# Performance work log

Measured on AMD Instinct MI355X. Metric: run time of the kernel, lower is better.

## Reference

```python
import jax, jax.numpy as jnp
import numpy as np

D = 1024
H = 16
DFF = 4096
EPS = 1e-5


def layernorm(x, g, b):
    m = jnp.mean(x, axis=-1, keepdims=True)
    v = jnp.var(x, axis=-1, keepdims=True)
    return (x - m) * jax.lax.rsqrt(v + EPS) * g + b


def setup_inputs() -> dict:
    key = jax.random.key(0)
    ks = jax.random.split(key, 6)
    B, T = 2, 2048
    s = 0.02
    return {
        "x": jax.random.normal(ks[0], (B, T, D), dtype=jnp.float32),
        "W_qkv": jax.random.normal(ks[1], (D, 3 * D), dtype=jnp.float32) * s,
        "W_proj": jax.random.normal(ks[2], (D, D), dtype=jnp.float32) * s,
        "W_fc1": jax.random.normal(ks[3], (D, DFF), dtype=jnp.float32) * s,
        "W_fc2": jax.random.normal(ks[4], (DFF, D), dtype=jnp.float32) * s,
        "ln1_g": jnp.ones((D,), jnp.float32),
        "ln1_b": jnp.zeros((D,), jnp.float32),
        "ln2_g": jnp.ones((D,), jnp.float32),
        "ln2_b": jnp.zeros((D,), jnp.float32),
    }


def reference(x, W_qkv, W_proj, W_fc1, W_fc2, ln1_g, ln1_b, ln2_g, ln2_b):
    B, T, C = x.shape
    hd = C // H

    # --- attention sublayer (pre-norm) ---
    h = layernorm(x, ln1_g, ln1_b)
    qkv = h @ W_qkv                                  # [B,T,3C]
    q, k, v = jnp.split(qkv, 3, axis=-1)
    q = q.reshape(B, T, H, hd).transpose(0, 2, 1, 3)  # [B,H,T,hd]
    k = k.reshape(B, T, H, hd).transpose(0, 2, 1, 3)
    v = v.reshape(B, T, H, hd).transpose(0, 2, 1, 3)
    att = jnp.einsum('bhqd,bhkd->bhqk', q, k) * (1.0 / np.sqrt(hd))
    causal = jnp.tril(jnp.ones((T, T), dtype=bool))
    att = jnp.where(causal, att, jnp.float32(-jnp.inf))
    att = jax.nn.softmax(att, axis=-1)
    y = jnp.einsum('bhqk,bhkd->bhqd', att, v)        # [B,H,T,hd]
    y = y.transpose(0, 2, 1, 3).reshape(B, T, C)
    x = x + y @ W_proj

    # --- MLP sublayer (pre-norm) ---
    h = layernorm(x, ln2_g, ln2_b)
    h = jax.nn.gelu(h @ W_fc1, approximate=False)
    x = x + h @ W_fc2
    return x
```

## Files before the change

kernel.cpp:

```cpp
#include <hip/hip_runtime.h>
#include <hip/hip_bf16.h>
#include <math.h>

typedef __bf16 bf16;
typedef __bf16 bf16x4 __attribute__((ext_vector_type(4)));
typedef __bf16 bf16x8 __attribute__((ext_vector_type(8)));
typedef float f32x4 __attribute__((ext_vector_type(4)));
typedef unsigned int u32;

#define MFMA_BF16(a, b, c) __builtin_amdgcn_mfma_f32_16x16x32_bf16(a, b, c, 0, 0, 0)
#define ASYNC16(g, l)                                                                   \
    __builtin_amdgcn_global_load_lds((const __attribute__((address_space(1))) u32*)(g), \
                                     (__attribute__((address_space(3))) u32*)(l), 16, 0, 0)

__global__ __launch_bounds__(256)
void transpose_cast(const float* __restrict__ in, bf16* __restrict__ out, int rows, int cols) {
    __shared__ float tile[32][33];
    const int tx = threadIdx.x, ty = threadIdx.y;
    const int c0 = blockIdx.x * 32, r0 = blockIdx.y * 32;
    #pragma unroll
    for (int j = 0; j < 4; j++)
        tile[ty + j * 8][tx] = in[(size_t)(r0 + ty + j * 8) * cols + c0 + tx];
    __syncthreads();
    #pragma unroll
    for (int j = 0; j < 4; j++)
        out[(size_t)(c0 + ty + j * 8) * rows + r0 + tx] = (bf16)tile[tx][ty + j * 8];
}

__global__ __launch_bounds__(256)
void transpose_v(const bf16* __restrict__ qkv, bf16* __restrict__ vt) {
    __shared__ bf16 tile[32][33];
    const int tx = threadIdx.x, ty = threadIdx.y;
    const int t0 = blockIdx.x * 32;
    const int d0 = blockIdx.y * 32;
    const int bh = blockIdx.z;
    const int b = bh >> 4, h = bh & 15;
    const bf16* src = qkv + (size_t)b * 2048 * 3072 + 2048 + h * 64;
    #pragma unroll
    for (int j = 0; j < 4; j++)
        tile[ty + j * 8][tx] = src[(size_t)(t0 + ty + j * 8) * 3072 + d0 + tx];
    __syncthreads();
    #pragma unroll
    for (int j = 0; j < 4; j++)
        vt[((size_t)bh * 64 + d0 + ty + j * 8) * 2048 + t0 + tx] = tile[tx][ty + j * 8];
}

__global__ __launch_bounds__(256)
void ln_kernel(const float* __restrict__ x, const float* __restrict__ g,
               const float* __restrict__ bb, bf16* __restrict__ out) {
    const int row = blockIdx.x, tid = threadIdx.x;
    const float4 v = reinterpret_cast<const float4*>(x)[(size_t)row * 256 + tid];
    float s = v.x + v.y + v.z + v.w;
    float sq = v.x * v.x + v.y * v.y + v.z * v.z + v.w * v.w;
    #pragma unroll
    for (int o = 32; o > 0; o >>= 1) { s += __shfl_xor(s, o); sq += __shfl_xor(sq, o); }
    __shared__ float ssum[4], ssq[4];
    const int wave = tid >> 6, lane = tid & 63;
    if (lane == 0) { ssum[wave] = s; ssq[wave] = sq; }
    __syncthreads();
    s = ssum[0] + ssum[1] + ssum[2] + ssum[3];
    sq = ssq[0] + ssq[1] + ssq[2] + ssq[3];
    const float mean = s * (1.0f / 1024.0f);
    const float var = sq * (1.0f / 1024.0f) - mean * mean;
    const float rstd = rsqrtf(var + 1e-5f);
    const float4 gv = reinterpret_cast<const float4*>(g)[tid];
    const float4 bv = reinterpret_cast<const float4*>(bb)[tid];
    bf16x4 o;
    o[0] = (bf16)((v.x - mean) * rstd * gv.x + bv.x);
    o[1] = (bf16)((v.y - mean) * rstd * gv.y + bv.y);
    o[2] = (bf16)((v.z - mean) * rstd * gv.z + bv.z);
    o[3] = (bf16)((v.w - mean) * rstd * gv.w + bv.w);
    reinterpret_cast<bf16x4*>(out)[(size_t)row * 256 + tid] = o;
}

__device__ __forceinline__ float gelu_fast(float v) {
    const float vv = v * v;
    const float u = v * (1.595769122f + 0.0713548162726f * vv);
    const float t = exp2f(u * -1.4426950408889634f);
    return v / (1.0f + t);
}

template <int EPI>
__global__ __launch_bounds__(512, 2)
void gemm256(const bf16* __restrict__ A, const bf16* __restrict__ Bt,
             bf16* __restrict__ outb, int M, int N, int K) {
    __shared__ bf16 As[2][2][2][128][32];
    __shared__ bf16 Bs[2][2][2][128][32];
    const int tid = threadIdx.x;
    const int wave = tid >> 6, lane = tid & 63;
    const int lm = lane & 15, lq = lane >> 4;
    const int wr = wave >> 2, wc = wave & 3;
    const int bm = blockIdx.y * 256, bn = blockIdx.x * 256;
    const int srow = lane >> 2;
    const int sg = (((lane & 3) ^ ((lane >> 3) & 3)) * 8);
    const int pco = (lq ^ ((lm >> 1) & 3)) * 8;

    f32x4 acc[8][4];
    #pragma unroll
    for (int i = 0; i < 8; i++)
        #pragma unroll
        for (int j = 0; j < 4; j++) acc[i][j] = (f32x4){0.f, 0.f, 0.f, 0.f};

    auto stageA = [&](int db, int kt) {
        #pragma unroll
        for (int L = 0; L < 2; L++) {
            const int g = wave * 2 + L, slab = g >> 3, rg = g & 7;
            #pragma unroll
            for (int h = 0; h < 2; h++)
                ASYNC16(A + (size_t)(bm + h * 128 + rg * 16 + srow) * K + kt + slab * 32 + sg,
                        &As[db][h][slab][rg * 16][0]);
        }
    };
    auto stageB = [&](int db, int kt) {
        #pragma unroll
        for (int L = 0; L < 2; L++) {
            const int g = wave * 2 + L, slab = g >> 3, rg = g & 7;
            #pragma unroll
            for (int h = 0; h < 2; h++)
                ASYNC16(Bt + (size_t)(bn + h * 128 + rg * 16 + srow) * K + kt + slab * 32 + sg,
                        &Bs[db][h][slab][rg * 16][0]);
        }
    };
    auto loadA = [&](int db, int mq, bf16x8 (&dst)[4][2]) {
        #pragma unroll
        for (int i = 0; i < 4; i++)
            #pragma unroll
            for (int kk = 0; kk < 2; kk++)
                dst[i][kk] = *reinterpret_cast<const bf16x8*>(
                    &As[db][wr][kk][(mq * 4 + i) * 16 + lm][pco]);
    };
    auto loadB = [&](int db, int bq, bf16x8 (&dst)[2][2]) {
        #pragma unroll
        for (int j = 0; j < 2; j++)
            #pragma unroll
            for (int kk = 0; kk < 2; kk++)
                dst[j][kk] = *reinterpret_cast<const bf16x8*>(
                    &Bs[db][wc >> 1][kk][(wc & 1) * 64 + (bq * 2 + j) * 16 + lm][pco]);
    };
    auto quad = [&](int mq, int bq, bf16x8 (&a)[4][2], bf16x8 (&b)[2][2]) {
        #pragma unroll
        for (int kk = 0; kk < 2; kk++)
            #pragma unroll
            for (int i = 0; i < 4; i++)
                #pragma unroll
                for (int j = 0; j < 2; j++)
                    acc[mq * 4 + i][bq * 2 + j] =
                        MFMA_BF16(a[i][kk], b[j][kk], acc[mq * 4 + i][bq * 2 + j]);
    };

#define PHASE_SYNC()                                         \
    __builtin_amdgcn_s_barrier();                            \
    asm volatile("s_waitcnt lgkmcnt(0)" ::: "memory");       \
    __builtin_amdgcn_sched_barrier(0)

    const int NT = K >> 6;
    stageB(0, 0);  stageA(0, 0);
    stageB(1, 64); stageA(1, 64);
    asm volatile("s_waitcnt vmcnt(8)" ::: "memory");
    __builtin_amdgcn_s_barrier();
    __builtin_amdgcn_sched_barrier(0);

    bf16x8 af[4][2], b0[2][2], b1[2][2];
    for (int t = 0; t < NT; ++t) {
        const int db = t & 1;
        const int kt2 = (t + 2) * 64;
        loadA(db, 0, af);
        loadB(db, 0, b0);
        PHASE_SYNC();
        __builtin_amdgcn_s_setprio(1);
        quad(0, 0, af, b0);
        __builtin_amdgcn_s_setprio(0);
        __builtin_amdgcn_s_barrier();
        loadB(db, 1, b1);
        PHASE_SYNC();
        __builtin_amdgcn_s_setprio(1);
        quad(0, 1, af, b1);
        __builtin_amdgcn_s_setprio(0);
        __builtin_amdgcn_s_barrier();
        loadA(db, 1, af);
        if (t + 2 < NT) stageB(db, kt2);
        PHASE_SYNC();
        __builtin_amdgcn_s_setprio(1);
        quad(1, 0, af, b0);
        __builtin_amdgcn_s_setprio(0);
        __builtin_amdgcn_s_barrier();
        if (t + 2 < NT) {
            stageA(db, kt2);
            asm volatile("s_waitcnt vmcnt(8)" ::: "memory");
        } else if (t + 1 < NT) {
            asm volatile("s_waitcnt vmcnt(0)" ::: "memory");
        }
        __builtin_amdgcn_s_barrier();
        __builtin_amdgcn_sched_barrier(0);
        __builtin_amdgcn_s_setprio(1);
        quad(1, 1, af, b1);
        __builtin_amdgcn_s_setprio(0);
        __builtin_amdgcn_s_barrier();
    }
#undef PHASE_SYNC

    const int r0 = bm + wr * 128, c0 = bn + wc * 64;
    #pragma unroll
    for (int mi = 0; mi < 8; mi++)
        #pragma unroll
        for (int ni = 0; ni < 4; ni++)
            #pragma unroll
            for (int e = 0; e < 4; e++) {
                const int row = r0 + mi * 16 + lq * 4 + e;
                const int col = c0 + ni * 16 + lm;
                const float v = acc[mi][ni][e];
                const size_t idx = (size_t)row * N + col;
                if (EPI == 0) outb[idx] = (bf16)v;
                else          outb[idx] = (bf16)gelu_fast(v);
            }
}

__global__ __launch_bounds__(256)
void gemm_bt64(const bf16* __restrict__ A, const bf16* __restrict__ Bt,
               const float* __restrict__ resid, float* __restrict__ outf,
               int M, int N, int K) {
    __shared__ bf16 As[2][128][64];
    __shared__ bf16 Bs[2][64][64];
    const int tid = threadIdx.x;
    const int wave = tid >> 6, lane = tid & 63;
    const int lm = lane & 15, lq = lane >> 4;
    const int wm = (wave >> 1) * 64, wn = (wave & 1) * 32;
    const int bm = blockIdx.y * 128, bn = blockIdx.x * 64;
    const int lr8 = lane >> 3;
    const int lg  = ((lane & 7) ^ lr8) * 8;
    const int sa  = lm & 7;
    int co[2];
    co[0] = (lq ^ sa) * 8;
    co[1] = ((lq ^ 4) ^ sa) * 8;
    f32x4 acc[4][2];
    #pragma unroll
    for (int i = 0; i < 4; i++)
        #pragma unroll
        for (int j = 0; j < 2; j++) acc[i][j] = (f32x4){0.f, 0.f, 0.f, 0.f};

    auto stage = [&](int bb, int kt) {
        #pragma unroll
        for (int s = 0; s < 4; s++)
            ASYNC16(A + (size_t)(bm + wave * 32 + s * 8 + lr8) * K + kt + lg, &As[bb][wave * 32 + s * 8][0]);
        #pragma unroll
        for (int s = 0; s < 2; s++)
            ASYNC16(Bt + (size_t)(bn + wave * 16 + s * 8 + lr8) * K + kt + lg, &Bs[bb][wave * 16 + s * 8][0]);
    };

    stage(0, 0);
    int cur = 0;
    for (int kt = 0; kt < K; kt += 64) {
        __syncthreads();
        if (kt + 64 < K) stage(cur ^ 1, kt + 64);
        bf16x8 af[2][4], bfr[2][2];
        #pragma unroll
        for (int kk = 0; kk < 2; kk++) {
            #pragma unroll
            for (int i = 0; i < 4; i++)
                af[kk][i] = *reinterpret_cast<const bf16x8*>(&As[cur][wm + i * 16 + lm][co[kk]]);
            #pragma unroll
            for (int j = 0; j < 2; j++)
                bfr[kk][j] = *reinterpret_cast<const bf16x8*>(&Bs[cur][wn + j * 16 + lm][co[kk]]);
        }
        #pragma unroll
        for (int kk = 0; kk < 2; kk++)
            #pragma unroll
            for (int i = 0; i < 4; i++)
                #pragma unroll
                for (int j = 0; j < 2; j++)
                    acc[i][j] = MFMA_BF16(af[kk][i], bfr[kk][j], acc[i][j]);
        cur ^= 1;
    }

    const int r0 = bm + wm, c0 = bn + wn;
    #pragma unroll
    for (int i = 0; i < 4; i++)
        #pragma unroll
        for (int j = 0; j < 2; j++)
            #pragma unroll
            for (int e = 0; e < 4; e++) {
                const int row = r0 + i * 16 + lq * 4 + e;
                const int col = c0 + j * 16 + lm;
                const size_t idx = (size_t)row * N + col;
                outf[idx] = resid[idx] + acc[i][j][e];
            }
}

__global__ __launch_bounds__(256)
void attn_kernel(const bf16* __restrict__ qkv, const bf16* __restrict__ vt,
                 bf16* __restrict__ y) {
    __shared__ bf16 Ks[64][68];
    __shared__ bf16 Vt[64][68];
    __shared__ bf16 Ps[4][16][68];
    const int tid = threadIdx.x, wave = tid >> 6, lane = tid & 63;
    const int lm = lane & 15, lq = lane >> 4;
    const int h = blockIdx.y, b = blockIdx.z;
    const size_t base = (size_t)b * 2048 * 3072;
    const bf16* Kbase = qkv + base + 1024 + h * 64;
    const bf16* Vbase = vt + ((size_t)(b * 16 + h) * 64) * 2048;
    const int skey = tid >> 3, sch = (tid & 7) * 8;
    const float k1 = 0.18033688011112042f;

    bf16x8 ones;
    #pragma unroll
    for (int j = 0; j < 8; j++) ones[j] = (lm == 0) ? (bf16)1.0f : (bf16)0.0f;

    for (int ph = 0; ph < 2; ph++) {
        const int qt = ph ? (int)blockIdx.x : 31 - (int)blockIdx.x;

        const int qrow = qt * 64 + wave * 16 + lm;
        const bf16* qp = qkv + base + (size_t)qrow * 3072 + h * 64 + lq * 8;
        bf16x8 aq0 = *reinterpret_cast<const bf16x8*>(qp);
        bf16x8 aq1 = *reinterpret_cast<const bf16x8*>(qp + 32);
        #pragma unroll
        for (int j = 0; j < 8; j++) {
            aq0[j] = (bf16)((float)aq0[j] * k1);
            aq1[j] = (bf16)((float)aq1[j] * k1);
        }

        f32x4 Oc[4], Ol;
        #pragma unroll
        for (int nt = 0; nt < 4; nt++) Oc[nt] = (f32x4){0.f, 0.f, 0.f, 0.f};
        Ol = (f32x4){0.f, 0.f, 0.f, 0.f};

        bf16x8 pk0, pk1, pv0, pv1;
        {
            const bf16* kp = Kbase + (size_t)skey * 3072 + sch;
            pk0 = *reinterpret_cast<const bf16x8*>(kp);
            pk1 = *reinterpret_cast<const bf16x8*>(kp + (size_t)32 * 3072);
            const bf16* vp = Vbase + (size_t)skey * 2048 + sch;
            pv0 = *reinterpret_cast<const bf16x8*>(vp);
            pv1 = *reinterpret_cast<const bf16x8*>(vp + (size_t)32 * 2048);
        }

        for (int kt2 = 0; kt2 <= qt; kt2++) {
            __syncthreads();
            *reinterpret_cast<bf16x8*>(&Ks[skey][sch])      = pk0;
            *reinterpret_cast<bf16x8*>(&Ks[skey + 32][sch]) = pk1;
            *reinterpret_cast<bf16x8*>(&Vt[skey][sch])      = pv0;
            *reinterpret_cast<bf16x8*>(&Vt[skey + 32][sch]) = pv1;
            __syncthreads();
            if (kt2 < qt) {
                const bf16* kp = Kbase + (size_t)((kt2 + 1) * 64 + skey) * 3072 + sch;
                pk0 = *reinterpret_cast<const bf16x8*>(kp);
                pk1 = *reinterpret_cast<const bf16x8*>(kp + (size_t)32 * 3072);
                const bf16* vp = Vbase + (size_t)skey * 2048 + (kt2 + 1) * 64 + sch;
                pv0 = *reinterpret_cast<const bf16x8*>(vp);
                pv1 = *reinterpret_cast<const bf16x8*>(vp + (size_t)32 * 2048);
            }

            f32x4 Sc[4];
            #pragma unroll
            for (int nt = 0; nt < 4; nt++) Sc[nt] = (f32x4){0.f, 0.f, 0.f, 0.f};
            #pragma unroll
            for (int nt = 0; nt < 4; nt++) {
                const bf16x8 bk0 = *reinterpret_cast<const bf16x8*>(&Ks[nt * 16 + lm][lq * 8]);
                const bf16x8 bk1 = *reinterpret_cast<const bf16x8*>(&Ks[nt * 16 + lm][32 + lq * 8]);
                Sc[nt] = MFMA_BF16(aq0, bk0, Sc[nt]);
                Sc[nt] = MFMA_BF16(aq1, bk1, Sc[nt]);
            }

            const int qb = wave * 16 + lq * 4;
            #pragma unroll
            for (int e = 0; e < 4; e++) {
                #pragma unroll
                for (int nt = 0; nt < 4; nt++) {
                    float sv = Sc[nt][e];
                    if (kt2 == qt && (nt * 16 + lm) > (qb + e)) sv = -1e30f;
                    Ps[wave][lq * 4 + e][nt * 16 + lm] = (bf16)exp2f(sv);
                }
            }

            const bf16x8 ap0 = *reinterpret_cast<const bf16x8*>(&Ps[wave][lm][lq * 8]);
            const bf16x8 ap1 = *reinterpret_cast<const bf16x8*>(&Ps[wave][lm][32 + lq * 8]);
            Ol = MFMA_BF16(ap0, ones, Ol);
            Ol = MFMA_BF16(ap1, ones, Ol);
            #pragma unroll
            for (int nt = 0; nt < 4; nt++) {
                const bf16x8 bv0 = *reinterpret_cast<const bf16x8*>(&Vt[nt * 16 + lm][lq * 8]);
                const bf16x8 bv1 = *reinterpret_cast<const bf16x8*>(&Vt[nt * 16 + lm][32 + lq * 8]);
                Oc[nt] = MFMA_BF16(ap0, bv0, Oc[nt]);
                Oc[nt] = MFMA_BF16(ap1, bv1, Oc[nt]);
            }
        }

        const int qrow0 = qt * 64 + wave * 16 + lq * 4;
        float inv[4];
        #pragma unroll
        for (int e = 0; e < 4; e++) inv[e] = 1.0f / __shfl(Ol[e], lane & 48);
        #pragma unroll
        for (int nt = 0; nt < 4; nt++)
            #pragma unroll
            for (int e = 0; e < 4; e++) {
                const int row = qrow0 + e;
                y[((size_t)b * 2048 + row) * 1024 + h * 64 + nt * 16 + lm] = (bf16)(Oc[nt][e] * inv[e]);
            }
    }
}

extern "C" void kernel_launch(void* const* d_in, const int* in_sizes, int n_in,
                              void* d_out, int out_size, void* d_ws, size_t ws_size,
                              hipStream_t stream) {
    const float* x     = (const float*)d_in[0];
    const float* Wqkv  = (const float*)d_in[1];
    const float* Wproj = (const float*)d_in[2];
    const float* Wfc1  = (const float*)d_in[3];
    const float* Wfc2  = (const float*)d_in[4];
    const float* ln1g  = (const float*)d_in[5];
    const float* ln1b  = (const float*)d_in[6];
    const float* ln2g  = (const float*)d_in[7];
    const float* ln2b  = (const float*)d_in[8];
    float* out = (float*)d_out;
    char* ws = (char*)d_ws;

    bf16*  Wqkvt  = (bf16*)(ws);
    bf16*  Wprojt = (bf16*)(ws + 6291456);
    bf16*  Wfc1t  = (bf16*)(ws + 8388608);
    bf16*  Wfc2t  = (bf16*)(ws + 16777216);
    bf16*  hb     = (bf16*)(ws + 25165824);
    bf16*  vt     = (bf16*)(ws + 25165824);
    bf16*  qkv    = (bf16*)(ws + 33554432);
    bf16*  yb     = (bf16*)(ws + 58720256);
    float* x1     = (float*)(ws + 67108864);
    bf16*  h3     = (bf16*)(ws + 33554432);

    const dim3 tb(32, 8);
    transpose_cast<<<dim3(96, 32), tb, 0, stream>>>(Wqkv, Wqkvt, 1024, 3072);
    transpose_cast<<<dim3(32, 32), tb, 0, stream>>>(Wproj, Wprojt, 1024, 1024);
    transpose_cast<<<dim3(128, 32), tb, 0, stream>>>(Wfc1, Wfc1t, 1024, 4096);
    transpose_cast<<<dim3(32, 128), tb, 0, stream>>>(Wfc2, Wfc2t, 4096, 1024);

    ln_kernel<<<dim3(4096), dim3(256), 0, stream>>>(x, ln1g, ln1b, hb);
    gemm256<0><<<dim3(12, 16), dim3(512), 0, stream>>>(hb, Wqkvt, qkv, 4096, 3072, 1024);
    transpose_v<<<dim3(64, 2, 32), tb, 0, stream>>>(qkv, vt);
    attn_kernel<<<dim3(16, 16, 2), dim3(256), 0, stream>>>(qkv, vt, yb);
    gemm_bt64<<<dim3(16, 32), dim3(256), 0, stream>>>(yb, Wprojt, x, x1, 4096, 1024, 1024);
    ln_kernel<<<dim3(4096), dim3(256), 0, stream>>>(x1, ln2g, ln2b, hb);
    gemm256<2><<<dim3(16, 16), dim3(512), 0, stream>>>(hb, Wfc1t, h3, 4096, 4096, 1024);
    gemm_bt64<<<dim3(16, 32), dim3(256), 0, stream>>>(h3, Wfc2t, x1, out, 4096, 1024, 4096);
}
```

Baseline: 343.3 us.

## Replace residual GEMM with 128x128 tile, K=32 steps and swizzled block order

The residual-add GEMMs (projection and fc2) move from a 128x64 tile with K-step 64 to a 128x128 tile with K-step 32. Each wave now computes a 64x64 sub-tile with 16 accumulators, which raises MFMA work per LDS fragment load. The grid halves to 256 workgroups, and block indices are remapped in groups of 8 (likely to improve L2 locality). The LDS swizzle is redone for the 32-wide rows. Fewer workgroups (256) on a large-CU GPU may leave compute units idle, and the shorter K step adds more barriers per unit of work.

```diff
diff --git a/kernel.cpp b/kernel.cpp
--- a/kernel.cpp
+++ b/kernel.cpp
@@ -216,59 +216,54 @@
 }
 
 __global__ __launch_bounds__(256)
-void gemm_bt64(const bf16* __restrict__ A, const bf16* __restrict__ Bt,
-               const float* __restrict__ resid, float* __restrict__ outf,
-               int M, int N, int K) {
-    __shared__ bf16 As[2][128][64];
-    __shared__ bf16 Bs[2][64][64];
+void gemm128r(const bf16* __restrict__ A, const bf16* __restrict__ Bt,
+              const float* __restrict__ resid, float* __restrict__ outf,
+              int M, int N, int K) {
+    __shared__ bf16 As[2][128][32];
+    __shared__ bf16 Bs[2][128][32];
     const int tid = threadIdx.x;
     const int wave = tid >> 6, lane = tid & 63;
     const int lm = lane & 15, lq = lane >> 4;
-    const int wm = (wave >> 1) * 64, wn = (wave & 1) * 32;
-    const int bm = blockIdx.y * 128, bn = blockIdx.x * 64;
-    const int lr8 = lane >> 3;
-    const int lg  = ((lane & 7) ^ lr8) * 8;
-    const int sa  = lm & 7;
-    int co[2];
-    co[0] = (lq ^ sa) * 8;
-    co[1] = ((lq ^ 4) ^ sa) * 8;
-    f32x4 acc[4][2];
+    const int wm = (wave >> 1) * 64, wn = (wave & 1) * 64;
+    const int nwg = gridDim.x * gridDim.y;
+    const int orig = blockIdx.x + gridDim.x * blockIdx.y;
+    const int cpx = nwg >> 3;
+    const int swz = (orig & 7) * cpx + (orig >> 3);
+    const int bx = swz % gridDim.x, by = swz / gridDim.x;
+    const int bm = by * 128, bn = bx * 128;
+    const int srow = lane >> 2;
+    const int sg = (((lane & 3) ^ ((lane >> 3) & 3)) * 8);
+    const int pco = (lq ^ ((lm >> 1) & 3)) * 8;
+    f32x4 acc[4][4];
     #pragma unroll
     for (int i = 0; i < 4; i++)
         #pragma unroll
-        for (int j = 0; j < 2; j++) acc[i][j] = (f32x4){0.f, 0.f, 0.f, 0.f};
+        for (int j = 0; j < 4; j++) acc[i][j] = (f32x4){0.f, 0.f, 0.f, 0.f};
 
     auto stage = [&](int bb, int kt) {
-        #pragma unroll
-        for (int s = 0; s < 4; s++)
-            ASYNC16(A + (size_t)(bm + wave * 32 + s * 8 + lr8) * K + kt + lg, &As[bb][wave * 32 + s * 8][0]);
-        #pragma unroll
-        for (int s = 0; s < 2; s++)
-            ASYNC16(Bt + (size_t)(bn + wave * 16 + s * 8 + lr8) * K + kt + lg, &Bs[bb][wave * 16 + s * 8][0]);
+        ASYNC16(A + (size_t)(bm + wave * 32 + srow) * K + kt + sg,      &As[bb][wave * 32][0]);
+        ASYNC16(A + (size_t)(bm + wave * 32 + 16 + srow) * K + kt + sg, &As[bb][wave * 32 + 16][0]);
+        ASYNC16(Bt + (size_t)(bn + wave * 32 + srow) * K + kt + sg,      &Bs[bb][wave * 32][0]);
+        ASYNC16(Bt + (size_t)(bn + wave * 32 + 16 + srow) * K + kt + sg, &Bs[bb][wave * 32 + 16][0]);
     };
 
     stage(0, 0);
     int cur = 0;
-    for (int kt = 0; kt < K; kt += 64) {
+    for (int kt = 0; kt < K; kt += 32) {
         __syncthreads();
-        if (kt + 64 < K) stage(cur ^ 1, kt + 64);
-        bf16x8 af[2][4], bfr[2][2];
-        #pragma unroll
-        for (int kk = 0; kk < 2; kk++) {
-            #pragma unroll
-            for (int i = 0; i < 4; i++)
-                af[kk][i] = *reinterpret_cast<const bf16x8*>(&As[cur][wm + i * 16 + lm][co[kk]]);
-            #pragma unroll
-            for (int j = 0; j < 2; j++)
-                bfr[kk][j] = *reinterpret_cast<const bf16x8*>(&Bs[cur][wn + j * 16 + lm][co[kk]]);
-        }
-        #pragma unroll
-        for (int kk = 0; kk < 2; kk++)
-            #pragma unroll
-            for (int i = 0; i < 4; i++)
-                #pragma unroll
-                for (int j = 0; j < 2; j++)
-                    acc[i][j] = MFMA_BF16(af[kk][i], bfr[kk][j], acc[i][j]);
+        if (kt + 32 < K) stage(cur ^ 1, kt + 32);
+        bf16x8 af[4], bfr[4];
+        #pragma unroll
+        for (int i = 0; i < 4; i++)
+            af[i] = *reinterpret_cast<const bf16x8*>(&As[cur][wm + i * 16 + lm][pco]);
+        #pragma unroll
+        for (int j = 0; j < 4; j++)
+            bfr[j] = *reinterpret_cast<const bf16x8*>(&Bs[cur][wn + j * 16 + lm][pco]);
+        #pragma unroll
+        for (int i = 0; i < 4; i++)
+            #pragma unroll
+            for (int j = 0; j < 4; j++)
+                acc[i][j] = MFMA_BF16(af[i], bfr[j], acc[i][j]);
         cur ^= 1;
     }
 
@@ -276,7 +271,7 @@
     #pragma unroll
     for (int i = 0; i < 4; i++)
         #pragma unroll
-        for (int j = 0; j < 2; j++)
+        for (int j = 0; j < 4; j++)
             #pragma unroll
             for (int e = 0; e < 4; e++) {
                 const int row = r0 + i * 16 + lq * 4 + e;
@@ -434,8 +429,8 @@
     gemm256<0><<<dim3(12, 16), dim3(512), 0, stream>>>(hb, Wqkvt, qkv, 4096, 3072, 1024);
     transpose_v<<<dim3(64, 2, 32), tb, 0, stream>>>(qkv, vt);
     attn_kernel<<<dim3(16, 16, 2), dim3(256), 0, stream>>>(qkv, vt, yb);
-    gemm_bt64<<<dim3(16, 32), dim3(256), 0, stream>>>(yb, Wprojt, x, x1, 4096, 1024, 1024);
+    gemm128r<<<dim3(8, 32), dim3(256), 0, stream>>>(yb, Wprojt, x, x1, 4096, 1024, 1024);
     ln_kernel<<<dim3(4096), dim3(256), 0, stream>>>(x1, ln2g, ln2b, hb);
     gemm256<2><<<dim3(16, 16), dim3(512), 0, stream>>>(hb, Wfc1t, h3, 4096, 4096, 1024);
-    gemm_bt64<<<dim3(16, 32), dim3(256), 0, stream>>>(h3, Wfc2t, x1, out, 4096, 1024, 4096);
-}
+    gemm128r<<<dim3(8, 32), dim3(256), 0, stream>>>(h3, Wfc2t, x1, out, 4096, 1024, 4096);
+}
```

Measured after the change: 366.2 us. +6.7%, slower.

## Replace residual GEMM with 128x128 triple-buffered ping-pong pipelined kernel

Applied to the files above, without the earlier changes.

Replaces the 128x64 double-buffered residual-add GEMM with a 128x128 tile, 512-thread kernel that keeps three LDS stages and splits each K-step into two half-phases. Barriers and explicit waitcnt calls interleave the async A/B loads with the MFMA work, and setprio raises priority during the MFMA bursts. The aim is to improve data reuse per block and hide global-load latency for the out-projection and FC2 GEMMs. The cost is more LDS per block (96KB), fewer blocks (256) on the chip, and fragile hand-tuned synchronisation.

```diff
diff --git a/kernel.cpp b/kernel.cpp
--- a/kernel.cpp
+++ b/kernel.cpp
@@ -215,17 +215,17 @@
             }
 }
 
-__global__ __launch_bounds__(256)
-void gemm_bt64(const bf16* __restrict__ A, const bf16* __restrict__ Bt,
-               const float* __restrict__ resid, float* __restrict__ outf,
-               int M, int N, int K) {
-    __shared__ bf16 As[2][128][64];
-    __shared__ bf16 Bs[2][64][64];
+__global__ __launch_bounds__(512, 2)
+void gemm128p(const bf16* __restrict__ A, const bf16* __restrict__ Bt,
+              const float* __restrict__ resid, float* __restrict__ outf,
+              int M, int N, int K) {
+    __shared__ bf16 As[3][128][64];
+    __shared__ bf16 Bs[3][128][64];
     const int tid = threadIdx.x;
     const int wave = tid >> 6, lane = tid & 63;
     const int lm = lane & 15, lq = lane >> 4;
-    const int wm = (wave >> 1) * 64, wn = (wave & 1) * 32;
-    const int bm = blockIdx.y * 128, bn = blockIdx.x * 64;
+    const int wm = (wave >> 2) * 64, wn = (wave & 3) * 32;
+    const int bm = blockIdx.y * 128, bn = blockIdx.x * 128;
     const int lr8 = lane >> 3;
     const int lg  = ((lane & 7) ^ lr8) * 8;
     const int sa  = lm & 7;
@@ -238,38 +238,73 @@
         #pragma unroll
         for (int j = 0; j < 2; j++) acc[i][j] = (f32x4){0.f, 0.f, 0.f, 0.f};
 
-    auto stage = [&](int bb, int kt) {
-        #pragma unroll
-        for (int s = 0; s < 4; s++)
-            ASYNC16(A + (size_t)(bm + wave * 32 + s * 8 + lr8) * K + kt + lg, &As[bb][wave * 32 + s * 8][0]);
-        #pragma unroll
-        for (int s = 0; s < 2; s++)
-            ASYNC16(Bt + (size_t)(bn + wave * 16 + s * 8 + lr8) * K + kt + lg, &Bs[bb][wave * 16 + s * 8][0]);
-    };
-
-    stage(0, 0);
-    int cur = 0;
-    for (int kt = 0; kt < K; kt += 64) {
-        __syncthreads();
-        if (kt + 64 < K) stage(cur ^ 1, kt + 64);
-        bf16x8 af[2][4], bfr[2][2];
-        #pragma unroll
-        for (int kk = 0; kk < 2; kk++) {
-            #pragma unroll
-            for (int i = 0; i < 4; i++)
-                af[kk][i] = *reinterpret_cast<const bf16x8*>(&As[cur][wm + i * 16 + lm][co[kk]]);
-            #pragma unroll
-            for (int j = 0; j < 2; j++)
-                bfr[kk][j] = *reinterpret_cast<const bf16x8*>(&Bs[cur][wn + j * 16 + lm][co[kk]]);
-        }
-        #pragma unroll
-        for (int kk = 0; kk < 2; kk++)
-            #pragma unroll
-            for (int i = 0; i < 4; i++)
-                #pragma unroll
-                for (int j = 0; j < 2; j++)
-                    acc[i][j] = MFMA_BF16(af[kk][i], bfr[kk][j], acc[i][j]);
-        cur ^= 1;
+    auto stageA = [&](int s, int kt) {
+        #pragma unroll
+        for (int c = 0; c < 2; c++)
+            ASYNC16(A + (size_t)(bm + (wave * 2 + c) * 8 + lr8) * K + kt + lg,
+                    &As[s][(wave * 2 + c) * 8][0]);
+    };
+    auto stageB = [&](int s, int kt) {
+        #pragma unroll
+        for (int c = 0; c < 2; c++)
+            ASYNC16(Bt + (size_t)(bn + (wave * 2 + c) * 8 + lr8) * K + kt + lg,
+                    &Bs[s][(wave * 2 + c) * 8][0]);
+    };
+
+    const int NT = K >> 6;
+    stageA(0, 0);  stageB(0, 0);
+    stageA(1, 64); stageB(1, 64);
+    asm volatile("s_waitcnt vmcnt(4)" ::: "memory");
+    __builtin_amdgcn_s_barrier();
+    __builtin_amdgcn_sched_barrier(0);
+
+    int s = 0;
+    for (int t = 0; t < NT; ++t) {
+        const int s2 = (s + 2 >= 3) ? s - 1 : s + 2;
+        const int kt2 = (t + 2) * 64;
+        bf16x8 a0[4], b0[2];
+        #pragma unroll
+        for (int mi = 0; mi < 4; mi++)
+            a0[mi] = *reinterpret_cast<const bf16x8*>(&As[s][wm + mi * 16 + lm][co[0]]);
+        #pragma unroll
+        for (int nj = 0; nj < 2; nj++)
+            b0[nj] = *reinterpret_cast<const bf16x8*>(&Bs[s][wn + nj * 16 + lm][co[0]]);
+        if (t + 2 < NT) stageA(s2, kt2);
+        __builtin_amdgcn_s_barrier();
+        asm volatile("s_waitcnt lgkmcnt(0)" ::: "memory");
+        __builtin_amdgcn_sched_barrier(0);
+        __builtin_amdgcn_s_setprio(1);
+        #pragma unroll
+        for (int mi = 0; mi < 4; mi++)
+            #pragma unroll
+            for (int nj = 0; nj < 2; nj++)
+                acc[mi][nj] = MFMA_BF16(a0[mi], b0[nj], acc[mi][nj]);
+        __builtin_amdgcn_s_setprio(0);
+        __builtin_amdgcn_s_barrier();
+        #pragma unroll
+        for (int mi = 0; mi < 4; mi++)
+            a0[mi] = *reinterpret_cast<const bf16x8*>(&As[s][wm + mi * 16 + lm][co[1]]);
+        #pragma unroll
+        for (int nj = 0; nj < 2; nj++)
+            b0[nj] = *reinterpret_cast<const bf16x8*>(&Bs[s][wn + nj * 16 + lm][co[1]]);
+        if (t + 2 < NT) {
+            stageB(s2, kt2);
+            asm volatile("s_waitcnt vmcnt(4)" ::: "memory");
+        } else if (t + 1 < NT) {
+            asm volatile("s_waitcnt vmcnt(0)" ::: "memory");
+        }
+        __builtin_amdgcn_s_barrier();
+        asm volatile("s_waitcnt lgkmcnt(0)" ::: "memory");
+        __builtin_amdgcn_sched_barrier(0);
+        __builtin_amdgcn_s_setprio(1);
+        #pragma unroll
+        for (int mi = 0; mi < 4; mi++)
+            #pragma unroll
+            for (int nj = 0; nj < 2; nj++)
+                acc[mi][nj] = MFMA_BF16(a0[mi], b0[nj], acc[mi][nj]);
+        __builtin_amdgcn_s_setprio(0);
+        __builtin_amdgcn_s_barrier();
+        s = (s == 2) ? 0 : s + 1;
     }
 
     const int r0 = bm + wm, c0 = bn + wn;
@@ -434,8 +469,8 @@
     gemm256<0><<<dim3(12, 16), dim3(512), 0, stream>>>(hb, Wqkvt, qkv, 4096, 3072, 1024);
     transpose_v<<<dim3(64, 2, 32), tb, 0, stream>>>(qkv, vt);
     attn_kernel<<<dim3(16, 16, 2), dim3(256), 0, stream>>>(qkv, vt, yb);
-    gemm_bt64<<<dim3(16, 32), dim3(256), 0, stream>>>(yb, Wprojt, x, x1, 4096, 1024, 1024);
+    gemm128p<<<dim3(8, 32), dim3(512), 0, stream>>>(yb, Wprojt, x, x1, 4096, 1024, 1024);
     ln_kernel<<<dim3(4096), dim3(256), 0, stream>>>(x1, ln2g, ln2b, hb);
     gemm256<2><<<dim3(16, 16), dim3(512), 0, stream>>>(hb, Wfc1t, h3, 4096, 4096, 1024);
-    gemm_bt64<<<dim3(16, 32), dim3(256), 0, stream>>>(h3, Wfc2t, x1, out, 4096, 1024, 4096);
-}
+    gemm128p<<<dim3(8, 32), dim3(512), 0, stream>>>(h3, Wfc2t, x1, out, 4096, 1024, 4096);
+}
```

Result: no change. 342.1 us (-0.3%).
